# Performance work log

Hardware: AMD Instinct MI355X
Metric: run time of the kernel (lower is better)

Reference implementation:

```python
import jax, jax.numpy as jnp
import numpy as np

HIDDEN = 1024
HEADS = 16
HEAD_SIZE = HIDDEN // HEADS


def setup_inputs() -> dict:
    key = jax.random.key(0)
    k0, k1, k2, k3 = jax.random.split(key, 4)
    scale = 1.0 / np.sqrt(HIDDEN)
    return {
        "input_data": jax.random.normal(k0, (4, 4096, HIDDEN), dtype=jnp.float32),
        "W0": jax.random.normal(k1, (HIDDEN, HIDDEN), dtype=jnp.float32) * scale,
        "W1": jax.random.normal(k2, (HIDDEN, HIDDEN), dtype=jnp.float32) * scale,
        "W2": jax.random.normal(k3, (HIDDEN, HIDDEN), dtype=jnp.float32) * scale,
    }


def reference(input_data, W0, W1, W2):
    b, s, _ = input_data.shape
    k, h = HEADS, HEAD_SIZE
    # torch.nn.Linear(bias=False): y = x @ W.T
    out = input_data @ W0.T          # [b, s, hidden]
    out1 = input_data @ W1.T
    out2 = input_data @ W2.T
    # reshape to heads; cummax over the sequence axis (axis=1 here, which
    # matches cummax(dim=2) on the permuted (b,k,s,h) layout in torch)
    out_h = out.reshape(b, s, k, h)
    out1_h = out1.reshape(b, s, k, h)
    cm = jax.lax.associative_scan(jnp.maximum, (out_h + out1_h) / jnp.sqrt(jnp.float32(h)), axis=1)
    cm = cm.reshape(b, s, k * h)
    out = (cm + out2) * cm + out1
    return out
```

## Files before the change

### kernel.cpp

```cpp
#include <hip/hip_runtime.h>
#include <cstdint>
#include <cstddef>

#define HIDDEN 1024
#define BATCH 4
#define SEQ 4096
#define M_ROWS (BATCH * SEQ)
#define K_DIM 1024
#define SUBCHUNK 32
#define NSUB (SEQ / SUBCHUNK)

typedef __bf16 bf16_t;
typedef __bf16 v8bf __attribute__((ext_vector_type(8)));
typedef float v4f __attribute__((ext_vector_type(4)));
typedef unsigned short us8 __attribute__((ext_vector_type(8)));

__device__ __forceinline__ unsigned short f32_to_bf16(float f) {
  unsigned int u = __float_as_uint(f);
  u += 0x7fffu + ((u >> 16) & 1u);
  return (unsigned short)(u >> 16);
}
__device__ __forceinline__ float bf16_to_f32(unsigned short u) {
  return __uint_as_float((unsigned int)u << 16);
}

__global__ void convert_kernel(const float* __restrict__ X,
                               const float* __restrict__ W0,
                               const float* __restrict__ W1,
                               const float* __restrict__ W2,
                               unsigned short* __restrict__ Xb,
                               unsigned short* __restrict__ Wb) {
  int bx = blockIdx.x;
  if (bx < 16384) {
    int i = bx * 256 + threadIdx.x;
    float4 f = ((const float4*)X)[i];
    ushort4 u;
    u.x = f32_to_bf16(f.x); u.y = f32_to_bf16(f.y);
    u.z = f32_to_bf16(f.z); u.w = f32_to_bf16(f.w);
    ((ushort4*)Xb)[i] = u;
  } else {
    int i = (bx - 16384) * 256 + threadIdx.x;
    int mat = i >> 18;
    int off = i & 0x3FFFF;
    float4 f;
    if (mat == 0) {
      float4 a = ((const float4*)W0)[off];
      float4 b = ((const float4*)W1)[off];
      f.x = (a.x + b.x) * 0.125f; f.y = (a.y + b.y) * 0.125f;
      f.z = (a.z + b.z) * 0.125f; f.w = (a.w + b.w) * 0.125f;
    } else {
      const float* src = (mat == 1) ? W1 : W2;
      f = ((const float4*)src)[off];
    }
    ushort4 u;
    u.x = f32_to_bf16(f.x); u.y = f32_to_bf16(f.y);
    u.z = f32_to_bf16(f.z); u.w = f32_to_bf16(f.w);
    ((ushort4*)Wb)[i] = u;
  }
}

__global__ __launch_bounds__(512, 2) void gemm_s_kernel(
    const bf16_t* __restrict__ A, const bf16_t* __restrict__ B,
    unsigned short* __restrict__ Lp, float* __restrict__ cmax) {
  extern __shared__ __align__(16) char smem[];

  const int tid = threadIdx.x;
  const int wave = tid >> 6;
  const int lane = tid & 63;
  const int quad = lane >> 4;
  const int r16 = lane & 15;
  const int wr = wave >> 2;
  const int wc = wave & 3;

  const int orig = (int)blockIdx.x;
  const int swz = (orig & 7) * 32 + (orig >> 3);
  const int bx = swz & 3;
  const int mt = swz >> 2;
  const int mtile0 = mt * 256;
  const int nbase = bx * 256;

  const int l3 = lane >> 3;
  const int lc = lane & 7;
  const size_t laneOff = (size_t)l3 * K_DIM + (size_t)((lc ^ l3) << 3);
  const bf16_t* Ag = A + (size_t)(mtile0 + wave * 8) * K_DIM + laneOff;
  const bf16_t* Bg = B + (size_t)(nbase + wave * 8) * K_DIM + laneOff;

  const int aRow = (wr * 128 + r16) * 128;
  const int bRow = (wc * 64 + r16) * 128;
  const int cxor = (r16 & 7) * 16;
  const int qx = quad * 16;

  v4f acc[8][4];
#pragma unroll
  for (int i = 0; i < 8; ++i)
#pragma unroll
    for (int j = 0; j < 4; ++j) acc[i][j] = (v4f)(0.0f);

  v8bf afr[4];
  v8bf bfr[4][2];

#define STG_A(d, q, kt) __builtin_amdgcn_global_load_lds( \
    (__attribute__((address_space(1))) void*)(Ag + (size_t)(q) * (64 * K_DIM) + (size_t)(kt) * 64), \
    (__attribute__((address_space(3))) void*)(smem + (d) * 32768 + (q) * 8192 + wave * 1024), 16, 0, 0)
#define STG_B(d, q, kt) __builtin_amdgcn_global_load_lds( \
    (__attribute__((address_space(1))) void*)(Bg + (size_t)(q) * (64 * K_DIM) + (size_t)(kt) * 64), \
    (__attribute__((address_space(3))) void*)(smem + 65536 + (d) * 32768 + (q) * 8192 + wave * 1024), 16, 0, 0)
#define LDA(d, i, kk) (*(const v8bf*)(smem + (d) * 32768 + aRow + (i) * 2048 + (((kk) * 64 + qx) ^ cxor)))
#define LDB(d, j, kk) (*(const v8bf*)(smem + 65536 + (d) * 32768 + bRow + (j) * 2048 + (((kk) * 64 + qx) ^ cxor)))
#define RD_A(d, ih, kk) { _Pragma("unroll") for (int ii = 0; ii < 4; ++ii) afr[ii] = LDA(d, (ih) * 4 + ii, kk); }
#define RD_B(d, kk) { _Pragma("unroll") for (int j = 0; j < 4; ++j) bfr[j][kk] = LDB(d, j, kk); }
#define MM(ih, kk) \
  __builtin_amdgcn_s_barrier(); \
  asm volatile("s_waitcnt lgkmcnt(0)" ::: "memory"); \
  __builtin_amdgcn_s_setprio(1); \
  { _Pragma("unroll") for (int ii = 0; ii < 4; ++ii) { _Pragma("unroll") for (int j = 0; j < 4; ++j) \
      acc[(ih) * 4 + ii][j] = __builtin_amdgcn_mfma_f32_16x16x32_bf16(afr[ii], bfr[j][(kk)], acc[(ih) * 4 + ii][j], 0, 0, 0); } } \
  __builtin_amdgcn_s_setprio(0);
#define BAR() __builtin_amdgcn_s_barrier()
#define WAITV(n) asm volatile("s_waitcnt vmcnt(" #n ")" ::: "memory")

  STG_A(0, 0, 0); STG_A(0, 1, 0); STG_A(0, 2, 0); STG_A(0, 3, 0);
  STG_B(0, 0, 0); STG_B(0, 1, 0); STG_B(0, 2, 0); STG_B(0, 3, 0);
  STG_A(1, 0, 1); STG_A(1, 2, 1); STG_B(1, 0, 1); STG_B(1, 1, 1);
  WAITV(4);
  BAR();

  for (int it = 0; it < 7; ++it) {
    const int t1 = 2 * it + 1, t2 = t1 + 1, t3 = t1 + 2;
    RD_A(0, 0, 0); RD_B(0, 0);
    STG_B(1, 2, t1); STG_B(1, 3, t1);
    MM(0, 0); BAR();
    RD_B(0, 1); RD_A(0, 0, 1);
    STG_A(1, 1, t1); STG_A(1, 3, t1);
    MM(0, 1); BAR();
    RD_A(0, 1, 0);
    STG_A(0, 0, t2); STG_A(0, 2, t2);
    MM(1, 0); BAR();
    RD_A(0, 1, 1);
    STG_B(0, 0, t2); STG_B(0, 1, t2);
    MM(1, 1); WAITV(4); BAR();
    RD_A(1, 0, 0); RD_B(1, 0);
    STG_B(0, 2, t2); STG_B(0, 3, t2);
    MM(0, 0); BAR();
    RD_B(1, 1); RD_A(1, 0, 1);
    STG_A(0, 1, t2); STG_A(0, 3, t2);
    MM(0, 1); BAR();
    RD_A(1, 1, 0);
    STG_A(1, 0, t3); STG_A(1, 2, t3);
    MM(1, 0); BAR();
    RD_A(1, 1, 1);
    STG_B(1, 0, t3); STG_B(1, 1, t3);
    MM(1, 1); WAITV(4); BAR();
  }
  RD_A(0, 0, 0); RD_B(0, 0);
  STG_B(1, 2, 15); STG_B(1, 3, 15);
  MM(0, 0); BAR();
  RD_B(0, 1); RD_A(0, 0, 1);
  STG_A(1, 1, 15); STG_A(1, 3, 15);
  MM(0, 1); BAR();
  RD_A(0, 1, 0); MM(1, 0); BAR();
  RD_A(0, 1, 1); MM(1, 1); WAITV(0); BAR();
  RD_A(1, 0, 0); RD_B(1, 0); MM(0, 0); BAR();
  RD_B(1, 1); RD_A(1, 0, 1); MM(0, 1); BAR();
  RD_A(1, 1, 0); MM(1, 0); BAR();
  RD_A(1, 1, 1); MM(1, 1);

#undef STG_A
#undef STG_B
#undef LDA
#undef LDB
#undef RD_A
#undef RD_B
#undef MM
#undef BAR
#undef WAITV

  const int ncol0 = bx * 256;
  const int bidx = mtile0 >> 12;
  const int sub0 = (mtile0 & 4095) >> 5;
#pragma unroll
  for (int s = 0; s < 4; ++s) {
#pragma unroll
    for (int j = 0; j < 4; ++j) {
      float c0[4], c1[4];
      c0[0] = acc[s * 2][j][0];
      c1[0] = acc[s * 2 + 1][j][0];
#pragma unroll
      for (int r = 1; r < 4; ++r) {
        c0[r] = fmaxf(c0[r - 1], acc[s * 2][j][r]);
        c1[r] = fmaxf(c1[r - 1], acc[s * 2 + 1][j][r]);
      }
      float t0 = c0[3], t1 = c1[3], u;
      u = __shfl_up(t0, 16); if (quad >= 1) t0 = fmaxf(t0, u);
      u = __shfl_up(t0, 32); if (quad >= 2) t0 = fmaxf(t0, u);
      u = __shfl_up(t1, 16); if (quad >= 1) t1 = fmaxf(t1, u);
      u = __shfl_up(t1, 32); if (quad >= 2) t1 = fmaxf(t1, u);
      float e0 = __shfl_up(t0, 16); if (quad == 0) e0 = -INFINITY;
      float e1 = __shfl_up(t1, 16); if (quad == 0) e1 = -INFINITY;
      float T0 = __shfl(t0, 48 + r16);
      float T1 = __shfl(t1, 48 + r16);
      int col = ncol0 + wc * 64 + j * 16 + r16;
      int rowb = mtile0 + wr * 128 + s * 32 + quad * 4;
#pragma unroll
      for (int r = 0; r < 4; ++r) {
        float L0 = fmaxf(c0[r], e0);
        float L1 = fmaxf(fmaxf(c1[r], e1), T0);
        Lp[(size_t)(rowb + r) * HIDDEN + col] = f32_to_bf16(L0);
        Lp[(size_t)(rowb + 16 + r) * HIDDEN + col] = f32_to_bf16(L1);
      }
      if (quad == 0) {
        int sub = sub0 + wr * 4 + s;
        cmax[((size_t)bidx * NSUB + sub) * HIDDEN + col] = fmaxf(T0, T1);
      }
    }
  }
}

__global__ void prefix_kernel(const float* __restrict__ cmax,
                              float* __restrict__ pmax) {
  int col = blockIdx.x * 256 + threadIdx.x;
  int b = blockIdx.y;
  const float* cp = cmax + (size_t)b * NSUB * HIDDEN + col;
  float* pp = pmax + (size_t)b * NSUB * HIDDEN + col;
  float run = -INFINITY;
#pragma unroll 1
  for (int s0 = 0; s0 < NSUB; s0 += 16) {
    float v[16];
#pragma unroll
    for (int i = 0; i < 16; ++i) v[i] = cp[(size_t)(s0 + i) * HIDDEN];
#pragma unroll
    for (int i = 0; i < 16; ++i) {
      pp[(size_t)(s0 + i) * HIDDEN] = run;
      run = fmaxf(run, v[i]);
    }
  }
}

__global__ __launch_bounds__(512, 2) void gemm_f_kernel(
    const bf16_t* __restrict__ A, const bf16_t* __restrict__ B,
    const unsigned short* __restrict__ Lp, const float* __restrict__ pmax,
    float* __restrict__ out) {
  extern __shared__ __align__(16) char smem[];

  const int tid = threadIdx.x;
  const int wave = tid >> 6;
  const int lane = tid & 63;
  const int quad = lane >> 4;
  const int r16 = lane & 15;
  const int wr = wave >> 2;
  const int wc = wave & 3;

  const int orig = (int)blockIdx.x;
  const int swz = (orig & 7) * 64 + (orig >> 3);
  const int mt = swz >> 3;
  const int nt = swz & 7;
  const int mtile0 = mt * 256;
  const int ncol0 = nt * 128;

  const int l3 = lane >> 3;
  const int lc = lane & 7;
  const size_t laneOff = (size_t)l3 * K_DIM + (size_t)((lc ^ l3) << 3);
  const bf16_t* Ag = A + (size_t)(mtile0 + wave * 8) * K_DIM + laneOff;
  const bf16_t* Bg1 = B + (size_t)(1024 + ncol0 + wave * 8) * K_DIM + laneOff;
  const bf16_t* Bg2 = B + (size_t)(2048 + ncol0 + wave * 8) * K_DIM + laneOff;

  const int aRow = (wr * 128 + r16) * 128;
  const int bRow = (wc * 32 + r16) * 128;
  const int cxor = (r16 & 7) * 16;
  const int qx = quad * 16;

  v4f acc1[8][2], acc2[8][2];
#pragma unroll
  for (int i = 0; i < 8; ++i)
#pragma unroll
    for (int j = 0; j < 2; ++j) { acc1[i][j] = (v4f)(0.0f); acc2[i][j] = (v4f)(0.0f); }

  v8bf afr[4];
  v8bf b1fr[2][2], b2fr[2][2];

#define STG2_A(d, q, kt) __builtin_amdgcn_global_load_lds( \
    (__attribute__((address_space(1))) void*)(Ag + (size_t)(q) * (64 * K_DIM) + (size_t)(kt) * 64), \
    (__attribute__((address_space(3))) void*)(smem + (d) * 32768 + (q) * 8192 + wave * 1024), 16, 0, 0)
#define STG2_B1(d, q, kt) __builtin_amdgcn_global_load_lds( \
    (__attribute__((address_space(1))) void*)(Bg1 + (size_t)(q) * (64 * K_DIM) + (size_t)(kt) * 64), \
    (__attribute__((address_space(3))) void*)(smem + 65536 + (d) * 32768 + (q) * 8192 + wave * 1024), 16, 0, 0)
#define STG2_B2(d, q, kt) __builtin_amdgcn_global_load_lds( \
    (__attribute__((address_space(1))) void*)(Bg2 + (size_t)(q) * (64 * K_DIM) + (size_t)(kt) * 64), \
    (__attribute__((address_space(3))) void*)(smem + 65536 + (d) * 32768 + 16384 + (q) * 8192 + wave * 1024), 16, 0, 0)
#define LDA2(d, i, kk) (*(const v8bf*)(smem + (d) * 32768 + aRow + (i) * 2048 + (((kk) * 64 + qx) ^ cxor)))
#define LDB21(d, j, kk) (*(const v8bf*)(smem + 65536 + (d) * 32768 + bRow + (j) * 2048 + (((kk) * 64 + qx) ^ cxor)))
#define LDB22(d, j, kk) (*(const v8bf*)(smem + 65536 + (d) * 32768 + 16384 + bRow + (j) * 2048 + (((kk) * 64 + qx) ^ cxor)))
#define RD2_A(d, ih, kk) { _Pragma("unroll") for (int ii = 0; ii < 4; ++ii) afr[ii] = LDA2(d, (ih) * 4 + ii, kk); }
#define RD2_B(d, kk) { _Pragma("unroll") for (int j = 0; j < 2; ++j) { b1fr[j][kk] = LDB21(d, j, kk); b2fr[j][kk] = LDB22(d, j, kk); } }
#define MM2(ih, kk) \
  __builtin_amdgcn_s_barrier(); \
  asm volatile("s_waitcnt lgkmcnt(0)" ::: "memory"); \
  __builtin_amdgcn_s_setprio(1); \
  { _Pragma("unroll") for (int ii = 0; ii < 4; ++ii) { _Pragma("unroll") for (int j = 0; j < 2; ++j) { \
      acc1[(ih) * 4 + ii][j] = __builtin_amdgcn_mfma_f32_16x16x32_bf16(afr[ii], b1fr[j][(kk)], acc1[(ih) * 4 + ii][j], 0, 0, 0); \
      acc2[(ih) * 4 + ii][j] = __builtin_amdgcn_mfma_f32_16x16x32_bf16(afr[ii], b2fr[j][(kk)], acc2[(ih) * 4 + ii][j], 0, 0, 0); } } } \
  __builtin_amdgcn_s_setprio(0);
#define BAR() __builtin_amdgcn_s_barrier()
#define WAITV(n) asm volatile("s_waitcnt vmcnt(" #n ")" ::: "memory")

  STG2_A(0, 0, 0); STG2_A(0, 1, 0); STG2_A(0, 2, 0); STG2_A(0, 3, 0);
  STG2_B1(0, 0, 0); STG2_B1(0, 1, 0); STG2_B2(0, 0, 0); STG2_B2(0, 1, 0);
  STG2_A(1, 0, 1); STG2_A(1, 2, 1); STG2_B1(1, 0, 1); STG2_B1(1, 1, 1);
  WAITV(4);
  BAR();

  for (int it = 0; it < 7; ++it) {
    const int t1 = 2 * it + 1, t2 = t1 + 1, t3 = t1 + 2;
    RD2_A(0, 0, 0); RD2_B(0, 0);
    STG2_B2(1, 0, t1); STG2_B2(1, 1, t1);
    MM2(0, 0); BAR();
    RD2_B(0, 1); RD2_A(0, 0, 1);
    STG2_A(1, 1, t1); STG2_A(1, 3, t1);
    MM2(0, 1); BAR();
    RD2_A(0, 1, 0);
    STG2_A(0, 0, t2); STG2_A(0, 2, t2);
    MM2(1, 0); BAR();
    RD2_A(0, 1, 1);
    STG2_B1(0, 0, t2); STG2_B1(0, 1, t2);
    MM2(1, 1); WAITV(4); BAR();
    RD2_A(1, 0, 0); RD2_B(1, 0);
    STG2_B2(0, 0, t2); STG2_B2(0, 1, t2);
    MM2(0, 0); BAR();
    RD2_B(1, 1); RD2_A(1, 0, 1);
    STG2_A(0, 1, t2); STG2_A(0, 3, t2);
    MM2(0, 1); BAR();
    RD2_A(1, 1, 0);
    STG2_A(1, 0, t3); STG2_A(1, 2, t3);
    MM2(1, 0); BAR();
    RD2_A(1, 1, 1);
    STG2_B1(1, 0, t3); STG2_B1(1, 1, t3);
    MM2(1, 1); WAITV(4); BAR();
  }
  RD2_A(0, 0, 0); RD2_B(0, 0);
  STG2_B2(1, 0, 15); STG2_B2(1, 1, 15);
  MM2(0, 0); BAR();
  RD2_B(0, 1); RD2_A(0, 0, 1);
  STG2_A(1, 1, 15); STG2_A(1, 3, 15);
  MM2(0, 1); BAR();
  RD2_A(0, 1, 0); MM2(1, 0); BAR();
  RD2_A(0, 1, 1); MM2(1, 1); WAITV(0); BAR();
  RD2_A(1, 0, 0); RD2_B(1, 0); MM2(0, 0); BAR();
  RD2_B(1, 1); RD2_A(1, 0, 1); MM2(0, 1); BAR();
  RD2_A(1, 1, 0); MM2(1, 0); BAR();
  RD2_A(1, 1, 1); MM2(1, 1);

#undef STG2_A
#undef STG2_B1
#undef STG2_B2
#undef LDA2
#undef LDB21
#undef LDB22
#undef RD2_A
#undef RD2_B
#undef MM2
#undef BAR
#undef WAITV

  const int bidx = mtile0 >> 12;
  const int sub0 = (mtile0 & 4095) >> 5;
#pragma unroll
  for (int i = 0; i < 8; ++i) {
    const int subr = sub0 + wr * 4 + (i >> 1);
#pragma unroll
    for (int j = 0; j < 2; ++j) {
      const int col = ncol0 + wc * 32 + j * 16 + r16;
      const float pm = pmax[((size_t)bidx * NSUB + subr) * HIDDEN + col];
      const int row0 = mtile0 + wr * 128 + i * 16 + quad * 4;
#pragma unroll
      for (int r = 0; r < 4; ++r) {
        size_t idx = (size_t)(row0 + r) * HIDDEN + col;
        float m = fmaxf(pm, bf16_to_f32(Lp[idx]));
        out[idx] = (m + acc2[i][j][r]) * m + acc1[i][j][r];
      }
    }
  }
}

extern "C" void kernel_launch(void* const* d_in, const int* in_sizes, int n_in,
                              void* d_out, int out_size, void* d_ws, size_t ws_size,
                              hipStream_t stream) {
  const float* X = (const float*)d_in[0];
  const float* W0 = (const float*)d_in[1];
  const float* W1 = (const float*)d_in[2];
  const float* W2 = (const float*)d_in[3];
  float* out = (float*)d_out;

  char* ws = (char*)d_ws;
  unsigned short* Xb = (unsigned short*)ws;
  unsigned short* Wb = (unsigned short*)(ws + 33554432);
  unsigned short* Lp = (unsigned short*)(ws + 33554432 + 6291456);
  float* cmax = (float*)(ws + 4 * 33554432 + 6291456);
  float* pmax = (float*)(ws + 4 * 33554432 + 6291456 + 2097152);

  convert_kernel<<<19456, 256, 0, stream>>>(X, W0, W1, W2, Xb, Wb);

  gemm_s_kernel<<<256, 512, 131072, stream>>>((const bf16_t*)Xb, (const bf16_t*)Wb,
                                              Lp, cmax);

  dim3 pgrid(4, BATCH);
  prefix_kernel<<<pgrid, 256, 0, stream>>>(cmax, pmax);

  gemm_f_kernel<<<512, 512, 131072, stream>>>((const bf16_t*)Xb, (const bf16_t*)Wb,
                                              Lp, pmax, out);
}
```

Baseline: 131.1 us.

## Double-buffer A fragments to overlap LDS reads with MFMA in both GEMMs

```diff
diff --git a/kernel.cpp b/kernel.cpp
--- a/kernel.cpp
+++ b/kernel.cpp
@@ -96,7 +96,7 @@
 #pragma unroll
     for (int j = 0; j < 4; ++j) acc[i][j] = (v4f)(0.0f);
 
-  v8bf afr[4];
+  v8bf afrE[4], afrO[4];
   v8bf bfr[4][2];
 
 #define STG_A(d, q, kt) __builtin_amdgcn_global_load_lds( \
@@ -107,14 +107,13 @@
     (__attribute__((address_space(3))) void*)(smem + 65536 + (d) * 32768 + (q) * 8192 + wave * 1024), 16, 0, 0)
 #define LDA(d, i, kk) (*(const v8bf*)(smem + (d) * 32768 + aRow + (i) * 2048 + (((kk) * 64 + qx) ^ cxor)))
 #define LDB(d, j, kk) (*(const v8bf*)(smem + 65536 + (d) * 32768 + bRow + (j) * 2048 + (((kk) * 64 + qx) ^ cxor)))
-#define RD_A(d, ih, kk) { _Pragma("unroll") for (int ii = 0; ii < 4; ++ii) afr[ii] = LDA(d, (ih) * 4 + ii, kk); }
+#define RD_AE(d, ih, kk) { _Pragma("unroll") for (int ii = 0; ii < 4; ++ii) afrE[ii] = LDA(d, (ih) * 4 + ii, kk); }
+#define RD_AO(d, ih, kk) { _Pragma("unroll") for (int ii = 0; ii < 4; ++ii) afrO[ii] = LDA(d, (ih) * 4 + ii, kk); }
 #define RD_B(d, kk) { _Pragma("unroll") for (int j = 0; j < 4; ++j) bfr[j][kk] = LDB(d, j, kk); }
-#define MM(ih, kk) \
-  __builtin_amdgcn_s_barrier(); \
-  asm volatile("s_waitcnt lgkmcnt(0)" ::: "memory"); \
+#define MMS(AF, ih, kk) \
   __builtin_amdgcn_s_setprio(1); \
   { _Pragma("unroll") for (int ii = 0; ii < 4; ++ii) { _Pragma("unroll") for (int j = 0; j < 4; ++j) \
-      acc[(ih) * 4 + ii][j] = __builtin_amdgcn_mfma_f32_16x16x32_bf16(afr[ii], bfr[j][(kk)], acc[(ih) * 4 + ii][j], 0, 0, 0); } } \
+      acc[(ih) * 4 + ii][j] = __builtin_amdgcn_mfma_f32_16x16x32_bf16(AF[ii], bfr[j][(kk)], acc[(ih) * 4 + ii][j], 0, 0, 0); } } \
   __builtin_amdgcn_s_setprio(0);
 #define BAR() __builtin_amdgcn_s_barrier()
 #define WAITV(n) asm volatile("s_waitcnt vmcnt(" #n ")" ::: "memory")
@@ -124,54 +123,74 @@
   STG_A(1, 0, 1); STG_A(1, 2, 1); STG_B(1, 0, 1); STG_B(1, 1, 1);
   WAITV(4);
   BAR();
+  RD_AE(0, 0, 0); RD_B(0, 0);
 
   for (int it = 0; it < 7; ++it) {
     const int t1 = 2 * it + 1, t2 = t1 + 1, t3 = t1 + 2;
-    RD_A(0, 0, 0); RD_B(0, 0);
     STG_B(1, 2, t1); STG_B(1, 3, t1);
-    MM(0, 0); BAR();
-    RD_B(0, 1); RD_A(0, 0, 1);
+    BAR();
+    RD_B(0, 1); RD_AO(0, 0, 1);
+    MMS(afrE, 0, 0); BAR();
     STG_A(1, 1, t1); STG_A(1, 3, t1);
-    MM(0, 1); BAR();
-    RD_A(0, 1, 0);
+    BAR();
+    RD_AE(0, 1, 0);
+    MMS(afrO, 0, 1); BAR();
     STG_A(0, 0, t2); STG_A(0, 2, t2);
-    MM(1, 0); BAR();
-    RD_A(0, 1, 1);
+    BAR();
+    RD_AO(0, 1, 1);
+    MMS(afrE, 1, 0); BAR();
     STG_B(0, 0, t2); STG_B(0, 1, t2);
-    MM(1, 1); WAITV(4); BAR();
-    RD_A(1, 0, 0); RD_B(1, 0);
+    BAR();
+    WAITV(4); BAR();
+    RD_AE(1, 0, 0); RD_B(1, 0);
+    MMS(afrO, 1, 1); BAR();
     STG_B(0, 2, t2); STG_B(0, 3, t2);
-    MM(0, 0); BAR();
-    RD_B(1, 1); RD_A(1, 0, 1);
+    BAR();
+    RD_B(1, 1); RD_AO(1, 0, 1);
+    MMS(afrE, 0, 0); BAR();
     STG_A(0, 1, t2); STG_A(0, 3, t2);
-    MM(0, 1); BAR();
-    RD_A(1, 1, 0);
+    BAR();
+    RD_AE(1, 1, 0);
+    MMS(afrO, 0, 1); BAR();
     STG_A(1, 0, t3); STG_A(1, 2, t3);
-    MM(1, 0); BAR();
-    RD_A(1, 1, 1);
+    BAR();
+    RD_AO(1, 1, 1);
+    MMS(afrE, 1, 0); BAR();
     STG_B(1, 0, t3); STG_B(1, 1, t3);
-    MM(1, 1); WAITV(4); BAR();
-  }
-  RD_A(0, 0, 0); RD_B(0, 0);
+    BAR();
+    WAITV(4); BAR();
+    RD_AE(0, 0, 0); RD_B(0, 0);
+    MMS(afrO, 1, 1); BAR();
+  }
   STG_B(1, 2, 15); STG_B(1, 3, 15);
-  MM(0, 0); BAR();
-  RD_B(0, 1); RD_A(0, 0, 1);
+  BAR();
+  RD_B(0, 1); RD_AO(0, 0, 1);
+  MMS(afrE, 0, 0); BAR();
   STG_A(1, 1, 15); STG_A(1, 3, 15);
-  MM(0, 1); BAR();
-  RD_A(0, 1, 0); MM(1, 0); BAR();
-  RD_A(0, 1, 1); MM(1, 1); WAITV(0); BAR();
-  RD_A(1, 0, 0); RD_B(1, 0); MM(0, 0); BAR();
-  RD_B(1, 1); RD_A(1, 0, 1); MM(0, 1); BAR();
-  RD_A(1, 1, 0); MM(1, 0); BAR();
-  RD_A(1, 1, 1); MM(1, 1);
+  BAR();
+  RD_AE(0, 1, 0);
+  MMS(afrO, 0, 1); BAR();
+  RD_AO(0, 1, 1);
+  MMS(afrE, 1, 0); BAR();
+  WAITV(0); BAR();
+  RD_AE(1, 0, 0); RD_B(1, 0);
+  MMS(afrO, 1, 1); BAR();
+  RD_B(1, 1); RD_AO(1, 0, 1);
+  MMS(afrE, 0, 0); BAR();
+  RD_AE(1, 1, 0);
+  MMS(afrO, 0, 1); BAR();
+  RD_AO(1, 1, 1);
+  MMS(afrE, 1, 0); BAR();
+  MMS(afrO, 1, 1);
 
 #undef STG_A
 #undef STG_B
 #undef LDA
 #undef LDB
-#undef RD_A
+#undef RD_AE
+#undef RD_AO
 #undef RD_B
-#undef MM
+#undef MMS
 #undef BAR
 #undef WAITV
 
@@ -275,7 +294,7 @@
 #pragma unroll
     for (int j = 0; j < 2; ++j) { acc1[i][j] = (v4f)(0.0f); acc2[i][j] = (v4f)(0.0f); }
 
-  v8bf afr[4];
+  v8bf afrE[4], afrO[4];
   v8bf b1fr[2][2], b2fr[2][2];
 
 #define STG2_A(d, q, kt) __builtin_amdgcn_global_load_lds( \
@@ -290,15 +309,14 @@
 #define LDA2(d, i, kk) (*(const v8bf*)(smem + (d) * 32768 + aRow + (i) * 2048 + (((kk) * 64 + qx) ^ cxor)))
 #define LDB21(d, j, kk) (*(const v8bf*)(smem + 65536 + (d) * 32768 + bRow + (j) * 2048 + (((kk) * 64 + qx) ^ cxor)))
 #define LDB22(d, j, kk) (*(const v8bf*)(smem + 65536 + (d) * 32768 + 16384 + bRow + (j) * 2048 + (((kk) * 64 + qx) ^ cxor)))
-#define RD2_A(d, ih, kk) { _Pragma("unroll") for (int ii = 0; ii < 4; ++ii) afr[ii] = LDA2(d, (ih) * 4 + ii, kk); }
+#define RD2_AE(d, ih, kk) { _Pragma("unroll") for (int ii = 0; ii < 4; ++ii) afrE[ii] = LDA2(d, (ih) * 4 + ii, kk); }
+#define RD2_AO(d, ih, kk) { _Pragma("unroll") for (int ii = 0; ii < 4; ++ii) afrO[ii] = LDA2(d, (ih) * 4 + ii, kk); }
 #define RD2_B(d, kk) { _Pragma("unroll") for (int j = 0; j < 2; ++j) { b1fr[j][kk] = LDB21(d, j, kk); b2fr[j][kk] = LDB22(d, j, kk); } }
-#define MM2(ih, kk) \
-  __builtin_amdgcn_s_barrier(); \
-  asm volatile("s_waitcnt lgkmcnt(0)" ::: "memory"); \
+#define MMS2(AF, ih, kk) \
   __builtin_amdgcn_s_setprio(1); \
   { _Pragma("unroll") for (int ii = 0; ii < 4; ++ii) { _Pragma("unroll") for (int j = 0; j < 2; ++j) { \
-      acc1[(ih) * 4 + ii][j] = __builtin_amdgcn_mfma_f32_16x16x32_bf16(afr[ii], b1fr[j][(kk)], acc1[(ih) * 4 + ii][j], 0, 0, 0); \
-      acc2[(ih) * 4 + ii][j] = __builtin_amdgcn_mfma_f32_16x16x32_bf16(afr[ii], b2fr[j][(kk)], acc2[(ih) * 4 + ii][j], 0, 0, 0); } } } \
+      acc1[(ih) * 4 + ii][j] = __builtin_amdgcn_mfma_f32_16x16x32_bf16(AF[ii], b1fr[j][(kk)], acc1[(ih) * 4 + ii][j], 0, 0, 0); \
+      acc2[(ih) * 4 + ii][j] = __builtin_amdgcn_mfma_f32_16x16x32_bf16(AF[ii], b2fr[j][(kk)], acc2[(ih) * 4 + ii][j], 0, 0, 0); } } } \
   __builtin_amdgcn_s_setprio(0);
 #define BAR() __builtin_amdgcn_s_barrier()
 #define WAITV(n) asm volatile("s_waitcnt vmcnt(" #n ")" ::: "memory")
@@ -308,46 +326,65 @@
   STG2_A(1, 0, 1); STG2_A(1, 2, 1); STG2_B1(1, 0, 1); STG2_B1(1, 1, 1);
   WAITV(4);
   BAR();
+  RD2_AE(0, 0, 0); RD2_B(0, 0);
 
   for (int it = 0; it < 7; ++it) {
     const int t1 = 2 * it + 1, t2 = t1 + 1, t3 = t1 + 2;
-    RD2_A(0, 0, 0); RD2_B(0, 0);
     STG2_B2(1, 0, t1); STG2_B2(1, 1, t1);
-    MM2(0, 0); BAR();
-    RD2_B(0, 1); RD2_A(0, 0, 1);
+    BAR();
+    RD2_B(0, 1); RD2_AO(0, 0, 1);
+    MMS2(afrE, 0, 0); BAR();
     STG2_A(1, 1, t1); STG2_A(1, 3, t1);
-    MM2(0, 1); BAR();
-    RD2_A(0, 1, 0);
+    BAR();
+    RD2_AE(0, 1, 0);
+    MMS2(afrO, 0, 1); BAR();
     STG2_A(0, 0, t2); STG2_A(0, 2, t2);
-    MM2(1, 0); BAR();
-    RD2_A(0, 1, 1);
+    BAR();
+    RD2_AO(0, 1, 1);
+    MMS2(afrE, 1, 0); BAR();
     STG2_B1(0, 0, t2); STG2_B1(0, 1, t2);
-    MM2(1, 1); WAITV(4); BAR();
-    RD2_A(1, 0, 0); RD2_B(1, 0);
+    BAR();
+    WAITV(4); BAR();
+    RD2_AE(1, 0, 0); RD2_B(1, 0);
+    MMS2(afrO, 1, 1); BAR();
     STG2_B2(0, 0, t2); STG2_B2(0, 1, t2);
-    MM2(0, 0); BAR();
-    RD2_B(1, 1); RD2_A(1, 0, 1);
+    BAR();
+    RD2_B(1, 1); RD2_AO(1, 0, 1);
+    MMS2(afrE, 0, 0); BAR();
     STG2_A(0, 1, t2); STG2_A(0, 3, t2);
-    MM2(0, 1); BAR();
-    RD2_A(1, 1, 0);
+    BAR();
+    RD2_AE(1, 1, 0);
+    MMS2(afrO, 0, 1); BAR();
     STG2_A(1, 0, t3); STG2_A(1, 2, t3);
-    MM2(1, 0); BAR();
-    RD2_A(1, 1, 1);
+    BAR();
+    RD2_AO(1, 1, 1);
+    MMS2(afrE, 1, 0); BAR();
     STG2_B1(1, 0, t3); STG2_B1(1, 1, t3);
-    MM2(1, 1); WAITV(4); BAR();
-  }
-  RD2_A(0, 0, 0); RD2_B(0, 0);
+    BAR();
+    WAITV(4); BAR();
+    RD2_AE(0, 0, 0); RD2_B(0, 0);
+    MMS2(afrO, 1, 1); BAR();
+  }
   STG2_B2(1, 0, 15); STG2_B2(1, 1, 15);
-  MM2(0, 0); BAR();
-  RD2_B(0, 1); RD2_A(0, 0, 1);
+  BAR();
+  RD2_B(0, 1); RD2_AO(0, 0, 1);
+  MMS2(afrE, 0, 0); BAR();
   STG2_A(1, 1, 15); STG2_A(1, 3, 15);
-  MM2(0, 1); BAR();
-  RD2_A(0, 1, 0); MM2(1, 0); BAR();
-  RD2_A(0, 1, 1); MM2(1, 1); WAITV(0); BAR();
-  RD2_A(1, 0, 0); RD2_B(1, 0); MM2(0, 0); BAR();
-  RD2_B(1, 1); RD2_A(1, 0, 1); MM2(0, 1); BAR();
-  RD2_A(1, 1, 0); MM2(1, 0); BAR();
-  RD2_A(1, 1, 1); MM2(1, 1);
+  BAR();
+  RD2_AE(0, 1, 0);
+  MMS2(afrO, 0, 1); BAR();
+  RD2_AO(0, 1, 1);
+  MMS2(afrE, 1, 0); BAR();
+  WAITV(0); BAR();
+  RD2_AE(1, 0, 0); RD2_B(1, 0);
+  MMS2(afrO, 1, 1); BAR();
+  RD2_B(1, 1); RD2_AO(1, 0, 1);
+  MMS2(afrE, 0, 0); BAR();
+  RD2_AE(1, 1, 0);
+  MMS2(afrO, 0, 1); BAR();
+  RD2_AO(1, 1, 1);
+  MMS2(afrE, 1, 0); BAR();
+  MMS2(afrO, 1, 1);
 
 #undef STG2_A
 #undef STG2_B1
@@ -355,9 +392,10 @@
 #undef LDA2
 #undef LDB21
 #undef LDB22
-#undef RD2_A
+#undef RD2_AE
+#undef RD2_AO
 #undef RD2_B
-#undef MM2
+#undef MMS2
 #undef BAR
 #undef WAITV
 
```

Result: no change. 131.3 us (median of 2 runs) (+0.2%).

## Switch both GEMM mainloops to 4-stage K=32 ring-buffer pipeline

Applied to the files above, without the earlier changes.

```diff
diff --git a/kernel.cpp b/kernel.cpp
--- a/kernel.cpp
+++ b/kernel.cpp
@@ -13,7 +13,6 @@
 typedef __bf16 bf16_t;
 typedef __bf16 v8bf __attribute__((ext_vector_type(8)));
 typedef float v4f __attribute__((ext_vector_type(4)));
-typedef unsigned short us8 __attribute__((ext_vector_type(8)));
 
 __device__ __forceinline__ unsigned short f32_to_bf16(float f) {
   unsigned int u = __float_as_uint(f);
@@ -59,6 +58,7 @@
   }
 }
 
+
 __global__ __launch_bounds__(512, 2) void gemm_s_kernel(
     const bf16_t* __restrict__ A, const bf16_t* __restrict__ B,
     unsigned short* __restrict__ Lp, float* __restrict__ cmax) {
@@ -79,16 +79,15 @@
   const int mtile0 = mt * 256;
   const int nbase = bx * 256;
 
-  const int l3 = lane >> 3;
-  const int lc = lane & 7;
-  const size_t laneOff = (size_t)l3 * K_DIM + (size_t)((lc ^ l3) << 3);
-  const bf16_t* Ag = A + (size_t)(mtile0 + wave * 8) * K_DIM + laneOff;
-  const bf16_t* Bg = B + (size_t)(nbase + wave * 8) * K_DIM + laneOff;
-
-  const int aRow = (wr * 128 + r16) * 128;
-  const int bRow = (wc * 64 + r16) * 128;
-  const int cxor = (r16 & 7) * 16;
-  const int qx = quad * 16;
+  const int sr = lane >> 2;
+  const int sc = lane & 3;
+  const size_t laneOff = (size_t)sr * K_DIM + (size_t)((sc ^ (sr & 3)) << 3);
+  const bf16_t* Ag = A + (size_t)(mtile0 + wave * 32) * K_DIM + laneOff;
+  const bf16_t* Bg = B + (size_t)(nbase + wave * 32) * K_DIM + laneOff;
+
+  const int aRowB = (wr * 128 + r16) * 64;
+  const int bRowB = (wc * 64 + r16) * 64;
+  const int kch = (quad ^ (r16 & 3)) << 4;
 
   v4f acc[8][4];
 #pragma unroll
@@ -97,81 +96,63 @@
     for (int j = 0; j < 4; ++j) acc[i][j] = (v4f)(0.0f);
 
   v8bf afr[4];
-  v8bf bfr[4][2];
-
-#define STG_A(d, q, kt) __builtin_amdgcn_global_load_lds( \
-    (__attribute__((address_space(1))) void*)(Ag + (size_t)(q) * (64 * K_DIM) + (size_t)(kt) * 64), \
-    (__attribute__((address_space(3))) void*)(smem + (d) * 32768 + (q) * 8192 + wave * 1024), 16, 0, 0)
-#define STG_B(d, q, kt) __builtin_amdgcn_global_load_lds( \
-    (__attribute__((address_space(1))) void*)(Bg + (size_t)(q) * (64 * K_DIM) + (size_t)(kt) * 64), \
-    (__attribute__((address_space(3))) void*)(smem + 65536 + (d) * 32768 + (q) * 8192 + wave * 1024), 16, 0, 0)
-#define LDA(d, i, kk) (*(const v8bf*)(smem + (d) * 32768 + aRow + (i) * 2048 + (((kk) * 64 + qx) ^ cxor)))
-#define LDB(d, j, kk) (*(const v8bf*)(smem + 65536 + (d) * 32768 + bRow + (j) * 2048 + (((kk) * 64 + qx) ^ cxor)))
-#define RD_A(d, ih, kk) { _Pragma("unroll") for (int ii = 0; ii < 4; ++ii) afr[ii] = LDA(d, (ih) * 4 + ii, kk); }
-#define RD_B(d, kk) { _Pragma("unroll") for (int j = 0; j < 4; ++j) bfr[j][kk] = LDB(d, j, kk); }
-#define MM(ih, kk) \
-  __builtin_amdgcn_s_barrier(); \
-  asm volatile("s_waitcnt lgkmcnt(0)" ::: "memory"); \
-  __builtin_amdgcn_s_setprio(1); \
-  { _Pragma("unroll") for (int ii = 0; ii < 4; ++ii) { _Pragma("unroll") for (int j = 0; j < 4; ++j) \
-      acc[(ih) * 4 + ii][j] = __builtin_amdgcn_mfma_f32_16x16x32_bf16(afr[ii], bfr[j][(kk)], acc[(ih) * 4 + ii][j], 0, 0, 0); } } \
-  __builtin_amdgcn_s_setprio(0);
+  v8bf bfr[4];
+
+#define STG_A(sb, st, jj) __builtin_amdgcn_global_load_lds( \
+    (__attribute__((address_space(1))) void*)(Ag + (size_t)(st) * 32 + (size_t)(jj) * (16 * K_DIM)), \
+    (__attribute__((address_space(3))) void*)(smem + (sb) * 16384 + wave * 2048 + (jj) * 1024), 16, 0, 0)
+#define STG_B(sb, st, jj) __builtin_amdgcn_global_load_lds( \
+    (__attribute__((address_space(1))) void*)(Bg + (size_t)(st) * 32 + (size_t)(jj) * (16 * K_DIM)), \
+    (__attribute__((address_space(3))) void*)(smem + 65536 + (sb) * 16384 + wave * 2048 + (jj) * 1024), 16, 0, 0)
+#define LDA(bf, i) (*(const v8bf*)(smem + (bf) * 16384 + aRowB + (i) * 1024 + kch))
+#define LDB(bf, j) (*(const v8bf*)(smem + 65536 + (bf) * 16384 + bRowB + (j) * 1024 + kch))
 #define BAR() __builtin_amdgcn_s_barrier()
 #define WAITV(n) asm volatile("s_waitcnt vmcnt(" #n ")" ::: "memory")
 
-  STG_A(0, 0, 0); STG_A(0, 1, 0); STG_A(0, 2, 0); STG_A(0, 3, 0);
-  STG_B(0, 0, 0); STG_B(0, 1, 0); STG_B(0, 2, 0); STG_B(0, 3, 0);
-  STG_A(1, 0, 1); STG_A(1, 2, 1); STG_B(1, 0, 1); STG_B(1, 1, 1);
-  WAITV(4);
+#define BODY(st, bf, DOSTG, WVW) { \
+    if (DOSTG) { STG_A((((st) + 3) & 3), (st) + 3, 0); STG_B((((st) + 3) & 3), (st) + 3, 0); } \
+    _Pragma("unroll") for (int j = 0; j < 4; ++j) bfr[j] = LDB(bf, j); \
+    _Pragma("unroll") for (int i = 0; i < 4; ++i) afr[i] = LDA(bf, i); \
+    __builtin_amdgcn_s_setprio(1); \
+    _Pragma("unroll") for (int i = 0; i < 4; ++i) \
+      _Pragma("unroll") for (int j = 0; j < 4; ++j) \
+        acc[i][j] = __builtin_amdgcn_mfma_f32_16x16x32_bf16(afr[i], bfr[j], acc[i][j], 0, 0, 0); \
+    __builtin_amdgcn_s_setprio(0); \
+    if (DOSTG) { STG_A((((st) + 3) & 3), (st) + 3, 1); STG_B((((st) + 3) & 3), (st) + 3, 1); } \
+    _Pragma("unroll") for (int i = 0; i < 4; ++i) afr[i] = LDA(bf, 4 + i); \
+    __builtin_amdgcn_s_setprio(1); \
+    _Pragma("unroll") for (int i = 0; i < 4; ++i) \
+      _Pragma("unroll") for (int j = 0; j < 4; ++j) \
+        acc[4 + i][j] = __builtin_amdgcn_mfma_f32_16x16x32_bf16(afr[i], bfr[j], acc[4 + i][j], 0, 0, 0); \
+    __builtin_amdgcn_s_setprio(0); \
+    WVW; BAR(); }
+
+#pragma unroll
+  for (int s = 0; s < 3; ++s) {
+    STG_A(s, s, 0); STG_B(s, s, 0);
+    STG_A(s, s, 1); STG_B(s, s, 1);
+  }
+  WAITV(8);
   BAR();
 
-  for (int it = 0; it < 7; ++it) {
-    const int t1 = 2 * it + 1, t2 = t1 + 1, t3 = t1 + 2;
-    RD_A(0, 0, 0); RD_B(0, 0);
-    STG_B(1, 2, t1); STG_B(1, 3, t1);
-    MM(0, 0); BAR();
-    RD_B(0, 1); RD_A(0, 0, 1);
-    STG_A(1, 1, t1); STG_A(1, 3, t1);
-    MM(0, 1); BAR();
-    RD_A(0, 1, 0);
-    STG_A(0, 0, t2); STG_A(0, 2, t2);
-    MM(1, 0); BAR();
-    RD_A(0, 1, 1);
-    STG_B(0, 0, t2); STG_B(0, 1, t2);
-    MM(1, 1); WAITV(4); BAR();
-    RD_A(1, 0, 0); RD_B(1, 0);
-    STG_B(0, 2, t2); STG_B(0, 3, t2);
-    MM(0, 0); BAR();
-    RD_B(1, 1); RD_A(1, 0, 1);
-    STG_A(0, 1, t2); STG_A(0, 3, t2);
-    MM(0, 1); BAR();
-    RD_A(1, 1, 0);
-    STG_A(1, 0, t3); STG_A(1, 2, t3);
-    MM(1, 0); BAR();
-    RD_A(1, 1, 1);
-    STG_B(1, 0, t3); STG_B(1, 1, t3);
-    MM(1, 1); WAITV(4); BAR();
-  }
-  RD_A(0, 0, 0); RD_B(0, 0);
-  STG_B(1, 2, 15); STG_B(1, 3, 15);
-  MM(0, 0); BAR();
-  RD_B(0, 1); RD_A(0, 0, 1);
-  STG_A(1, 1, 15); STG_A(1, 3, 15);
-  MM(0, 1); BAR();
-  RD_A(0, 1, 0); MM(1, 0); BAR();
-  RD_A(0, 1, 1); MM(1, 1); WAITV(0); BAR();
-  RD_A(1, 0, 0); RD_B(1, 0); MM(0, 0); BAR();
-  RD_B(1, 1); RD_A(1, 0, 1); MM(0, 1); BAR();
-  RD_A(1, 1, 0); MM(1, 0); BAR();
-  RD_A(1, 1, 1); MM(1, 1);
-
+#pragma unroll 1
+  for (int g = 0; g < 7; ++g) {
+    const int s0 = g * 4;
+    BODY(s0 + 0, 0, 1, WAITV(8));
+    BODY(s0 + 1, 1, 1, WAITV(8));
+    BODY(s0 + 2, 2, 1, WAITV(8));
+    BODY(s0 + 3, 3, 1, WAITV(8));
+  }
+  BODY(28, 0, 1, WAITV(8));
+  BODY(29, 1, 0, WAITV(4));
+  BODY(30, 2, 0, WAITV(0));
+  BODY(31, 3, 0, );
+
+#undef BODY
 #undef STG_A
 #undef STG_B
 #undef LDA
 #undef LDB
-#undef RD_A
-#undef RD_B
-#undef MM
 #undef BAR
 #undef WAITV
 
@@ -257,17 +238,16 @@
   const int mtile0 = mt * 256;
   const int ncol0 = nt * 128;
 
-  const int l3 = lane >> 3;
-  const int lc = lane & 7;
-  const size_t laneOff = (size_t)l3 * K_DIM + (size_t)((lc ^ l3) << 3);
-  const bf16_t* Ag = A + (size_t)(mtile0 + wave * 8) * K_DIM + laneOff;
-  const bf16_t* Bg1 = B + (size_t)(1024 + ncol0 + wave * 8) * K_DIM + laneOff;
-  const bf16_t* Bg2 = B + (size_t)(2048 + ncol0 + wave * 8) * K_DIM + laneOff;
-
-  const int aRow = (wr * 128 + r16) * 128;
-  const int bRow = (wc * 32 + r16) * 128;
-  const int cxor = (r16 & 7) * 16;
-  const int qx = quad * 16;
+  const int sr = lane >> 2;
+  const int sc = lane & 3;
+  const size_t laneOff = (size_t)sr * K_DIM + (size_t)((sc ^ (sr & 3)) << 3);
+  const bf16_t* Ag = A + (size_t)(mtile0 + wave * 32) * K_DIM + laneOff;
+  const bf16_t* Bg1 = B + (size_t)(1024 + ncol0 + wave * 16) * K_DIM + laneOff;
+  const bf16_t* Bg2 = B + (size_t)(2048 + ncol0 + wave * 16) * K_DIM + laneOff;
+
+  const int aRowB = (wr * 128 + r16) * 64;
+  const int bRowB = (wc * 32 + r16) * 64;
+  const int kch = (quad ^ (r16 & 3)) << 4;
 
   v4f acc1[8][2], acc2[8][2];
 #pragma unroll
@@ -276,88 +256,71 @@
     for (int j = 0; j < 2; ++j) { acc1[i][j] = (v4f)(0.0f); acc2[i][j] = (v4f)(0.0f); }
 
   v8bf afr[4];
-  v8bf b1fr[2][2], b2fr[2][2];
-
-#define STG2_A(d, q, kt) __builtin_amdgcn_global_load_lds( \
-    (__attribute__((address_space(1))) void*)(Ag + (size_t)(q) * (64 * K_DIM) + (size_t)(kt) * 64), \
-    (__attribute__((address_space(3))) void*)(smem + (d) * 32768 + (q) * 8192 + wave * 1024), 16, 0, 0)
-#define STG2_B1(d, q, kt) __builtin_amdgcn_global_load_lds( \
-    (__attribute__((address_space(1))) void*)(Bg1 + (size_t)(q) * (64 * K_DIM) + (size_t)(kt) * 64), \
-    (__attribute__((address_space(3))) void*)(smem + 65536 + (d) * 32768 + (q) * 8192 + wave * 1024), 16, 0, 0)
-#define STG2_B2(d, q, kt) __builtin_amdgcn_global_load_lds( \
-    (__attribute__((address_space(1))) void*)(Bg2 + (size_t)(q) * (64 * K_DIM) + (size_t)(kt) * 64), \
-    (__attribute__((address_space(3))) void*)(smem + 65536 + (d) * 32768 + 16384 + (q) * 8192 + wave * 1024), 16, 0, 0)
-#define LDA2(d, i, kk) (*(const v8bf*)(smem + (d) * 32768 + aRow + (i) * 2048 + (((kk) * 64 + qx) ^ cxor)))
-#define LDB21(d, j, kk) (*(const v8bf*)(smem + 65536 + (d) * 32768 + bRow + (j) * 2048 + (((kk) * 64 + qx) ^ cxor)))
-#define LDB22(d, j, kk) (*(const v8bf*)(smem + 65536 + (d) * 32768 + 16384 + bRow + (j) * 2048 + (((kk) * 64 + qx) ^ cxor)))
-#define RD2_A(d, ih, kk) { _Pragma("unroll") for (int ii = 0; ii < 4; ++ii) afr[ii] = LDA2(d, (ih) * 4 + ii, kk); }
-#define RD2_B(d, kk) { _Pragma("unroll") for (int j = 0; j < 2; ++j) { b1fr[j][kk] = LDB21(d, j, kk); b2fr[j][kk] = LDB22(d, j, kk); } }
-#define MM2(ih, kk) \
-  __builtin_amdgcn_s_barrier(); \
-  asm volatile("s_waitcnt lgkmcnt(0)" ::: "memory"); \
-  __builtin_amdgcn_s_setprio(1); \
-  { _Pragma("unroll") for (int ii = 0; ii < 4; ++ii) { _Pragma("unroll") for (int j = 0; j < 2; ++j) { \
-      acc1[(ih) * 4 + ii][j] = __builtin_amdgcn_mfma_f32_16x16x32_bf16(afr[ii], b1fr[j][(kk)], acc1[(ih) * 4 + ii][j], 0, 0, 0); \
-      acc2[(ih) * 4 + ii][j] = __builtin_amdgcn_mfma_f32_16x16x32_bf16(afr[ii], b2fr[j][(kk)], acc2[(ih) * 4 + ii][j], 0, 0, 0); } } } \
-  __builtin_amdgcn_s_setprio(0);
+  v8bf b1fr[2], b2fr[2];
+
+#define STG2_A(sb, st, jj) __builtin_amdgcn_global_load_lds( \
+    (__attribute__((address_space(1))) void*)(Ag + (size_t)(st) * 32 + (size_t)(jj) * (16 * K_DIM)), \
+    (__attribute__((address_space(3))) void*)(smem + (sb) * 16384 + wave * 2048 + (jj) * 1024), 16, 0, 0)
+#define STG2_B1(sb, st) __builtin_amdgcn_global_load_lds( \
+    (__attribute__((address_space(1))) void*)(Bg1 + (size_t)(st) * 32), \
+    (__attribute__((address_space(3))) void*)(smem + 65536 + (sb) * 16384 + wave * 1024), 16, 0, 0)
+#define STG2_B2(sb, st) __builtin_amdgcn_global_load_lds( \
+    (__attribute__((address_space(1))) void*)(Bg2 + (size_t)(st) * 32), \
+    (__attribute__((address_space(3))) void*)(smem + 65536 + (sb) * 16384 + 8192 + wave * 1024), 16, 0, 0)
+#define LDA2(bf, i) (*(const v8bf*)(smem + (bf) * 16384 + aRowB + (i) * 1024 + kch))
+#define LDB1(bf, j) (*(const v8bf*)(smem + 65536 + (bf) * 16384 + bRowB + (j) * 1024 + kch))
+#define LDB2(bf, j) (*(const v8bf*)(smem + 65536 + (bf) * 16384 + 8192 + bRowB + (j) * 1024 + kch))
 #define BAR() __builtin_amdgcn_s_barrier()
 #define WAITV(n) asm volatile("s_waitcnt vmcnt(" #n ")" ::: "memory")
 
-  STG2_A(0, 0, 0); STG2_A(0, 1, 0); STG2_A(0, 2, 0); STG2_A(0, 3, 0);
-  STG2_B1(0, 0, 0); STG2_B1(0, 1, 0); STG2_B2(0, 0, 0); STG2_B2(0, 1, 0);
-  STG2_A(1, 0, 1); STG2_A(1, 2, 1); STG2_B1(1, 0, 1); STG2_B1(1, 1, 1);
-  WAITV(4);
+#define BODY2(st, bf, DOSTG, WVW) { \
+    if (DOSTG) { STG2_A((((st) + 3) & 3), (st) + 3, 0); STG2_B1((((st) + 3) & 3), (st) + 3); } \
+    _Pragma("unroll") for (int j = 0; j < 2; ++j) { b1fr[j] = LDB1(bf, j); b2fr[j] = LDB2(bf, j); } \
+    _Pragma("unroll") for (int i = 0; i < 4; ++i) afr[i] = LDA2(bf, i); \
+    __builtin_amdgcn_s_setprio(1); \
+    _Pragma("unroll") for (int i = 0; i < 4; ++i) \
+      _Pragma("unroll") for (int j = 0; j < 2; ++j) { \
+        acc1[i][j] = __builtin_amdgcn_mfma_f32_16x16x32_bf16(afr[i], b1fr[j], acc1[i][j], 0, 0, 0); \
+        acc2[i][j] = __builtin_amdgcn_mfma_f32_16x16x32_bf16(afr[i], b2fr[j], acc2[i][j], 0, 0, 0); } \
+    __builtin_amdgcn_s_setprio(0); \
+    if (DOSTG) { STG2_A((((st) + 3) & 3), (st) + 3, 1); STG2_B2((((st) + 3) & 3), (st) + 3); } \
+    _Pragma("unroll") for (int i = 0; i < 4; ++i) afr[i] = LDA2(bf, 4 + i); \
+    __builtin_amdgcn_s_setprio(1); \
+    _Pragma("unroll") for (int i = 0; i < 4; ++i) \
+      _Pragma("unroll") for (int j = 0; j < 2; ++j) { \
+        acc1[4 + i][j] = __builtin_amdgcn_mfma_f32_16x16x32_bf16(afr[i], b1fr[j], acc1[4 + i][j], 0, 0, 0); \
+        acc2[4 + i][j] = __builtin_amdgcn_mfma_f32_16x16x32_bf16(afr[i], b2fr[j], acc2[4 + i][j], 0, 0, 0); } \
+    __builtin_amdgcn_s_setprio(0); \
+    WVW; BAR(); }
+
+#pragma unroll
+  for (int s = 0; s < 3; ++s) {
+    STG2_A(s, s, 0); STG2_B1(s, s);
+    STG2_A(s, s, 1); STG2_B2(s, s);
+  }
+  WAITV(8);
   BAR();
 
-  for (int it = 0; it < 7; ++it) {
-    const int t1 = 2 * it + 1, t2 = t1 + 1, t3 = t1 + 2;
-    RD2_A(0, 0, 0); RD2_B(0, 0);
-    STG2_B2(1, 0, t1); STG2_B2(1, 1, t1);
-    MM2(0, 0); BAR();
-    RD2_B(0, 1); RD2_A(0, 0, 1);
-    STG2_A(1, 1, t1); STG2_A(1, 3, t1);
-    MM2(0, 1); BAR();
-    RD2_A(0, 1, 0);
-    STG2_A(0, 0, t2); STG2_A(0, 2, t2);
-    MM2(1, 0); BAR();
-    RD2_A(0, 1, 1);
-    STG2_B1(0, 0, t2); STG2_B1(0, 1, t2);
-    MM2(1, 1); WAITV(4); BAR();
-    RD2_A(1, 0, 0); RD2_B(1, 0);
-    STG2_B2(0, 0, t2); STG2_B2(0, 1, t2);
-    MM2(0, 0); BAR();
-    RD2_B(1, 1); RD2_A(1, 0, 1);
-    STG2_A(0, 1, t2); STG2_A(0, 3, t2);
-    MM2(0, 1); BAR();
-    RD2_A(1, 1, 0);
-    STG2_A(1, 0, t3); STG2_A(1, 2, t3);
-    MM2(1, 0); BAR();
-    RD2_A(1, 1, 1);
-    STG2_B1(1, 0, t3); STG2_B1(1, 1, t3);
-    MM2(1, 1); WAITV(4); BAR();
-  }
-  RD2_A(0, 0, 0); RD2_B(0, 0);
-  STG2_B2(1, 0, 15); STG2_B2(1, 1, 15);
-  MM2(0, 0); BAR();
-  RD2_B(0, 1); RD2_A(0, 0, 1);
-  STG2_A(1, 1, 15); STG2_A(1, 3, 15);
-  MM2(0, 1); BAR();
-  RD2_A(0, 1, 0); MM2(1, 0); BAR();
-  RD2_A(0, 1, 1); MM2(1, 1); WAITV(0); BAR();
-  RD2_A(1, 0, 0); RD2_B(1, 0); MM2(0, 0); BAR();
-  RD2_B(1, 1); RD2_A(1, 0, 1); MM2(0, 1); BAR();
-  RD2_A(1, 1, 0); MM2(1, 0); BAR();
-  RD2_A(1, 1, 1); MM2(1, 1);
-
+#pragma unroll 1
+  for (int g = 0; g < 7; ++g) {
+    const int s0 = g * 4;
+    BODY2(s0 + 0, 0, 1, WAITV(8));
+    BODY2(s0 + 1, 1, 1, WAITV(8));
+    BODY2(s0 + 2, 2, 1, WAITV(8));
+    BODY2(s0 + 3, 3, 1, WAITV(8));
+  }
+  BODY2(28, 0, 1, WAITV(8));
+  BODY2(29, 1, 0, WAITV(4));
+  BODY2(30, 2, 0, WAITV(0));
+  BODY2(31, 3, 0, );
+
+#undef BODY2
 #undef STG2_A
 #undef STG2_B1
 #undef STG2_B2
 #undef LDA2
-#undef LDB21
-#undef LDB22
-#undef RD2_A
-#undef RD2_B
-#undef MM2
+#undef LDB1
+#undef LDB2
 #undef BAR
 #undef WAITV
 
```

Result: slower. 137.9 us (+5.2%).
